# Optimization experiments

Hardware: AMD Instinct MI355X
Metric: run time of the kernel (lower is better)

Reference implementation:

```python
import jax, jax.numpy as jnp
import numpy as np

N_NODES = 50000
N_EDGES = 800000
D_IN = 96
D_HID = 96
N_CLASSES = 10
N_LAYERS = 3
BN_EPS = 1e-5


def setup_inputs() -> dict:
    key = jax.random.key(0)
    ks = jax.random.split(key, 10)
    x = jax.random.normal(ks[0], (N_NODES, D_IN), dtype=jnp.float32)
    edge_index = jax.random.randint(ks[1], (2, N_EDGES), 0, N_NODES, dtype=jnp.int64)
    s = 1.0 / np.sqrt(D_HID)
    # stacked per-layer params (in_channels == hidden_channels == 96)
    w_neigh = jax.random.normal(ks[2], (N_LAYERS, D_HID, D_HID), dtype=jnp.float32) * s
    w_self = jax.random.normal(ks[3], (N_LAYERS, D_HID, D_HID), dtype=jnp.float32) * s
    bias = jnp.zeros((N_LAYERS, D_HID), dtype=jnp.float32)
    bn_gamma = jnp.ones((N_LAYERS, D_HID), dtype=jnp.float32)
    bn_beta = jnp.zeros((N_LAYERS, D_HID), dtype=jnp.float32)
    clf_w = jax.random.normal(ks[4], (D_HID, N_CLASSES), dtype=jnp.float32) * s
    clf_b = jnp.zeros((N_CLASSES,), dtype=jnp.float32)
    return {"x": x, "edge_index": edge_index, "w_neigh": w_neigh,
            "w_self": w_self, "bias": bias, "bn_gamma": bn_gamma,
            "bn_beta": bn_beta, "clf_w": clf_w, "clf_b": clf_b}


def reference(x, edge_index, w_neigh, w_self, bias, bn_gamma, bn_beta, clf_w, clf_b):
    n = x.shape[0]
    src, dst = edge_index[0], edge_index[1]
    # in-degree per dst node (mean aggregation denominator), zero-deg -> 1
    deg = jax.ops.segment_sum(jnp.ones((src.shape[0],), x.dtype), dst, num_segments=n)
    inv_deg = (1.0 / jnp.maximum(deg, 1.0))[:, None]  # [N,1]
    h = x
    for i in range(N_LAYERS):
        # SAGEConv: mean-aggregate neighbor features, then lin_l(agg) + lin_r(self)
        agg = jax.ops.segment_sum(h[src], dst, num_segments=n) * inv_deg  # [N,D]
        h = agg @ w_neigh[i] + h @ w_self[i] + bias[i]
        # BatchNorm over nodes (batch statistics), then ReLU; dropout = identity (eval)
        mu = jnp.mean(h, axis=0)
        var = jnp.var(h, axis=0)
        h = (h - mu) * jax.lax.rsqrt(var + BN_EPS) * bn_gamma[i] + bn_beta[i]
        h = jax.nn.relu(h)
    return h @ clf_w + clf_b  # [N, num_classes]
```

## Files before the change

### kernel.cpp

```cpp
#include <hip/hip_runtime.h>

#define NN 50000
#define NE 800000
#define D 96
#define NL 3
#define NC 10
#define BN_EPS 1e-5f
#define INV_N (1.0f / (float)NN)
#define NB 196
#define CAP 6144
#define EPB 2048
#define NREP 16
#define WPAD 200
#define AGGU 16
#define CASTB ((NN * D / 4 + 255) / 256)
#define PREPWB ((NL * D * 192 + 255) / 256)

typedef short bf16x8 __attribute__((ext_vector_type(8)));
typedef unsigned short u16x8 __attribute__((ext_vector_type(8)));
typedef float f32x4 __attribute__((ext_vector_type(4)));

__device__ __forceinline__ unsigned short f2b(float x) {
    unsigned int u = __float_as_uint(x);
    unsigned int r = (u + 0x7fffu + ((u >> 16) & 1u)) >> 16;
    return (unsigned short)r;
}
__device__ __forceinline__ float blo(unsigned int u) { return __uint_as_float(u << 16); }
__device__ __forceinline__ float bhi(unsigned int u) { return __uint_as_float(u & 0xffff0000u); }
__device__ __forceinline__ float b2f(short s) {
    return __uint_as_float(((unsigned int)(unsigned short)s) << 16);
}
__device__ __forceinline__ unsigned int pk2(float lo, float hi) {
    return ((unsigned int)f2b(lo)) | (((unsigned int)f2b(hi)) << 16);
}

__device__ __forceinline__ int edge_at(const void* idx, int is64, long long pos) {
    if (is64) return (int)((const long long*)idx)[pos];
    return ((const int*)idx)[pos];
}

__global__ void __launch_bounds__(256) prep_kernel(
        const float* __restrict__ x, unsigned short* __restrict__ xb,
        const float* __restrict__ wn, const float* __restrict__ ws,
        unsigned short* __restrict__ wt,
        const int* __restrict__ words, int* __restrict__ flag,
        int* __restrict__ cnt, float* __restrict__ stats) {
    int b = blockIdx.x;
    int t = threadIdx.x;
    if (b < CASTB) {
        int i = b * 256 + t;
        if (i < NN * D / 4) {
            float4 v = ((const float4*)x)[i];
            ushort4 o;
            o.x = f2b(v.x); o.y = f2b(v.y); o.z = f2b(v.z); o.w = f2b(v.w);
            ((ushort4*)xb)[i] = o;
        }
        return;
    }
    if (b < CASTB + PREPWB) {
        int i = (b - CASTB) * 256 + t;
        if (i < NL * D * 192) {
            int k = i % 192;
            int col = (i / 192) % D;
            int l = i / (192 * D);
            float v = (k < D) ? wn[(size_t)l * D * D + k * D + col]
                              : ws[(size_t)l * D * D + (k - D) * D + col];
            wt[((size_t)l * D + col) * WPAD + k] = f2b(v);
        }
        return;
    }
    __shared__ int any_nz;
    if (t == 0) any_nz = 0;
    __syncthreads();
    if (words[2 * t + 1] != 0) atomicOr(&any_nz, 1);
    __syncthreads();
    if (t == 0) *flag = any_nz ? 0 : 1;
    if (t < NB) cnt[t] = 0;
    for (int i = t; i < NL * NREP * 2 * D; i += 256) stats[i] = 0.f;
}

__global__ void __launch_bounds__(256) bin_kernel(
        const void* __restrict__ idx, const int* __restrict__ flag,
        int* __restrict__ cnt, unsigned int* __restrict__ binned, int E) {
    __shared__ int hist[256];
    __shared__ int gbase[256];
    __shared__ unsigned int pk[EPB];
    __shared__ unsigned char bkt[EPB];
    int t = threadIdx.x;
    int base = blockIdx.x * EPB;
    int is64 = *flag;
    hist[t] = 0;
    __syncthreads();
    #pragma unroll
    for (int j = 0; j < 8; ++j) {
        int i = t + j * 256;
        int e = base + i;
        if (e < E) {
            int s = edge_at(idx, is64, e);
            int d = edge_at(idx, is64, (long long)E + e);
            int b = d >> 8;
            bkt[i] = (unsigned char)b;
            pk[i] = ((unsigned int)s << 8) | (unsigned int)(d & 255);
            atomicAdd(&hist[b], 1);
        } else {
            bkt[i] = 0xFF;
        }
    }
    __syncthreads();
    int h = hist[t];
    int gb = 0;
    if (t < NB && h > 0) gb = atomicAdd(&cnt[t], h);
    gbase[t] = gb;
    hist[t] = 0;
    __syncthreads();
    #pragma unroll
    for (int j = 0; j < 8; ++j) {
        int i = t + j * 256;
        int b = bkt[i];
        if (b != 0xFF) {
            int loc = atomicAdd(&hist[b], 1);
            int pos = gbase[b] + loc;
            if (pos < CAP) binned[(size_t)b * CAP + pos] = pk[i];
        }
    }
}

__global__ void __launch_bounds__(256) fill_bucket_kernel(
        const unsigned int* __restrict__ binned, const int* __restrict__ cnt,
        int* __restrict__ row_ptr, float* __restrict__ inv_deg,
        int* __restrict__ csr_src) {
    __shared__ int sexcl[256];
    __shared__ int deg_l[256];
    __shared__ int wsum[4];
    __shared__ int lds_csr[CAP];
    int b = blockIdx.x;
    int t = threadIdx.x;
    int lane = t & 63, w = t >> 6;
    {
        int v = (t < NB) ? cnt[t] : 0;
        int x = v;
        #pragma unroll
        for (int off = 1; off < 64; off <<= 1) {
            int y = __shfl_up(x, off);
            if (lane >= off) x += y;
        }
        if (lane == 63) wsum[w] = x;
        __syncthreads();
        if (t == 0) {
            int r = 0;
            #pragma unroll
            for (int i = 0; i < 4; ++i) { int tt = wsum[i]; wsum[i] = r; r += tt; }
        }
        __syncthreads();
        sexcl[t] = x - v + wsum[w];
        __syncthreads();
    }
    int base = sexcl[b];
    int count = cnt[b]; if (count > CAP) count = CAP;
    int n0 = b << 8;
    deg_l[t] = 0;
    __syncthreads();
    const unsigned int* reg = binned + (size_t)b * CAP;
    for (int i = t; i < count; i += 256) atomicAdd(&deg_l[reg[i] & 255], 1);
    __syncthreads();
    int v = deg_l[t];
    int x = v;
    #pragma unroll
    for (int off = 1; off < 64; off <<= 1) {
        int y = __shfl_up(x, off);
        if (lane >= off) x += y;
    }
    if (lane == 63) wsum[w] = x;
    __syncthreads();
    if (t == 0) {
        int r = 0;
        #pragma unroll
        for (int i = 0; i < 4; ++i) { int tt = wsum[i]; wsum[i] = r; r += tt; }
    }
    __syncthreads();
    int excl = x - v + wsum[w];
    int node = n0 + t;
    if (node < NN) {
        row_ptr[node] = base + excl;
        inv_deg[node] = 1.0f / (float)(v > 0 ? v : 1);
    }
    if (b == 0 && t == 0) row_ptr[NN] = NE;
    deg_l[t] = excl;
    __syncthreads();
    for (int i = t; i < count; i += 256) {
        unsigned int pkv = reg[i];
        int loc = atomicAdd(&deg_l[pkv & 255], 1);
        lds_csr[loc] = (int)(pkv >> 8);
    }
    __syncthreads();
    for (int i = t; i < count; i += 256) csr_src[base + i] = lds_csr[i];
}

__global__ void bn_coef_kernel(const float* __restrict__ stats,
                               const float* __restrict__ gamma,
                               const float* __restrict__ beta,
                               float* __restrict__ scsh) {
    int f = threadIdx.x;
    if (f >= D) return;
    float s = 0.f, q = 0.f;
    #pragma unroll
    for (int r = 0; r < NREP; ++r) {
        s += stats[r * 2 * D + f];
        q += stats[r * 2 * D + D + f];
    }
    float mu = s * INV_N;
    float va = q * INV_N - mu * mu;
    float sc = rsqrtf(va + BN_EPS) * gamma[f];
    scsh[f] = sc;
    scsh[D + f] = beta[f] - mu * sc;
}

__global__ void agg_kernel(const unsigned short* __restrict__ hb,
                           const int* __restrict__ row_ptr,
                           const int* __restrict__ csr_src,
                           const float* __restrict__ inv_deg,
                           unsigned short* __restrict__ aggb,
                           const float* __restrict__ scsh_in,
                           int use_bn, int n) {
    int gid = blockIdx.x * blockDim.x + threadIdx.x;
    int node = gid >> 6;
    int lane = gid & 63;
    if (node >= n) return;
    bool act = lane < 48;
    float sc0 = 1.f, sh0 = 0.f, sc1 = 1.f, sh1 = 0.f;
    float lo = use_bn ? 0.f : -3.0e38f;
    if (use_bn && act) {
        float2 scp = *(const float2*)(scsh_in + lane * 2);
        float2 shp = *(const float2*)(scsh_in + D + lane * 2);
        sc0 = scp.x; sc1 = scp.y; sh0 = shp.x; sh1 = shp.y;
    }
    int beg = row_ptr[node], end = row_ptr[node + 1];
    float a0 = 0.f, a1 = 0.f, b0 = 0.f, b1 = 0.f;
    float c0 = 0.f, c1 = 0.f, d0 = 0.f, d1 = 0.f;

    int e = beg;
    int sidx[AGGU];
    #pragma unroll
    for (int j = 0; j < AGGU; ++j) sidx[j] = (e + j < end) ? csr_src[e + j] : -1;
    while (e < end) {
        int enext = e + AGGU;
        int snext[AGGU];
        #pragma unroll
        for (int j = 0; j < AGGU; ++j)
            snext[j] = (enext + j < end) ? csr_src[enext + j] : -1;
        unsigned int u[AGGU];
        #pragma unroll
        for (int j = 0; j < AGGU; ++j) {
            int s = sidx[j];
            u[j] = (s >= 0 && act)
                 ? *(const unsigned int*)(hb + (size_t)s * D + lane * 2) : 0u;
        }
        #pragma unroll
        for (int j = 0; j < AGGU; ++j) {
            if (sidx[j] >= 0) {
                float x0 = fmaxf(fmaf(blo(u[j]), sc0, sh0), lo);
                float x1 = fmaxf(fmaf(bhi(u[j]), sc1, sh1), lo);
                if ((j & 3) == 0) { a0 += x0; a1 += x1; }
                else if ((j & 3) == 1) { b0 += x0; b1 += x1; }
                else if ((j & 3) == 2) { c0 += x0; c1 += x1; }
                else { d0 += x0; d1 += x1; }
            }
        }
        #pragma unroll
        for (int j = 0; j < AGGU; ++j) sidx[j] = snext[j];
        e = enext;
    }
    a0 = (a0 + b0) + (c0 + d0);
    a1 = (a1 + b1) + (c1 + d1);
    if (act) {
        float idg = inv_deg[node];
        *(unsigned int*)(aggb + (size_t)node * D + lane * 2) = pk2(a0 * idg, a1 * idg);
    }
}

__global__ void __launch_bounds__(256) mfma_gemm_kernel(
        const unsigned short* __restrict__ aggb,
        const unsigned short* __restrict__ hb,
        const unsigned short* __restrict__ wt,
        const float* __restrict__ bias,
        unsigned short* __restrict__ hout,
        float* __restrict__ stats,
        const float* __restrict__ scsh_in,
        int use_bn, int n) {
    __shared__ float red[4][192];
    __shared__ float sSC[D];
    __shared__ float sSH[D];
    __shared__ unsigned short sW[D][WPAD];
    int tid = threadIdx.x;
    int wave = tid >> 6;
    int lane = tid & 63;
    int m16 = lane & 15;
    int hi = lane >> 4;
    int rbase = blockIdx.x * 64 + wave * 16;

    int arow = rbase + m16;
    int arowc = arow < n ? arow : n - 1;
    const unsigned short* ap = aggb + (size_t)arowc * D + hi * 8;
    const unsigned short* hp = hb + (size_t)arowc * D + hi * 8;
    bf16x8 A[6], H[3];
    #pragma unroll
    for (int kk = 0; kk < 3; ++kk) A[kk] = *reinterpret_cast<const bf16x8*>(ap + kk * 32);
    #pragma unroll
    for (int kk = 0; kk < 3; ++kk) H[kk] = *reinterpret_cast<const bf16x8*>(hp + kk * 32);

    #pragma unroll
    for (int c = 0; c < 9; ++c) {
        int i = tid + c * 256;
        int col = i / 24, seg = i % 24;
        *reinterpret_cast<u16x8*>(&sW[col][seg * 8]) =
            *reinterpret_cast<const u16x8*>(wt + (size_t)col * WPAD + seg * 8);
    }

    if (use_bn && tid < D) {
        sSC[tid] = scsh_in[tid];
        sSH[tid] = scsh_in[D + tid];
    }
    __syncthreads();

    #pragma unroll
    for (int kk = 0; kk < 3; ++kk) {
        if (use_bn) {
            bf16x8 T;
            #pragma unroll
            for (int j = 0; j < 8; ++j) {
                int f = kk * 32 + hi * 8 + j;
                float v = fmaxf(fmaf(b2f(H[kk][j]), sSC[f], sSH[f]), 0.f);
                T[j] = (short)f2b(v);
            }
            A[3 + kk] = T;
        } else {
            A[3 + kk] = H[kk];
        }
    }

    f32x4 acc[6];
    #pragma unroll
    for (int nn = 0; nn < 6; ++nn) acc[nn] = (f32x4){0.f, 0.f, 0.f, 0.f};
    #pragma unroll
    for (int nn = 0; nn < 6; ++nn) {
        int col = nn * 16 + m16;
        #pragma unroll
        for (int kk = 0; kk < 6; ++kk) {
            bf16x8 B = *reinterpret_cast<const bf16x8*>(&sW[col][kk * 32 + hi * 8]);
            acc[nn] = __builtin_amdgcn_mfma_f32_16x16x32_bf16(A[kk], B, acc[nn], 0, 0, 0);
        }
    }

    #pragma unroll
    for (int nn = 0; nn < 6; ++nn) {
        int f = nn * 16 + m16;
        float bv = bias[f];
        float s = 0.f, q = 0.f;
        #pragma unroll
        for (int r = 0; r < 4; ++r) {
            int rrow = rbase + hi * 4 + r;
            float v = acc[nn][r] + bv;
            if (rrow < n) {
                hout[(size_t)rrow * D + f] = f2b(v);
                s += v;
                q += v * v;
            }
        }
        s += __shfl_xor(s, 16); q += __shfl_xor(q, 16);
        s += __shfl_xor(s, 32); q += __shfl_xor(q, 32);
        if (lane < 16) {
            red[wave][f] = s;
            red[wave][96 + f] = q;
        }
    }
    __syncthreads();
    if (tid < 192) {
        float t = red[0][tid] + red[1][tid] + red[2][tid] + red[3][tid];
        atomicAdd(&stats[(blockIdx.x & (NREP - 1)) * 2 * D + tid], t);
    }
}

__global__ void clf_kernel(const unsigned short* __restrict__ h,
                           const float* __restrict__ W,
                           const float* __restrict__ b,
                           const float* __restrict__ scsh_in,
                           float* __restrict__ out, int n) {
    __shared__ float sW[D * NC];
    __shared__ float sB[NC];
    __shared__ float sSC[D];
    __shared__ float sSH[D];
    int tid = threadIdx.x;
    for (int i = tid; i < D * NC; i += blockDim.x) sW[i] = W[i];
    if (tid < NC) sB[tid] = b[tid];
    if (tid < D) {
        sSC[tid] = scsh_in[tid];
        sSH[tid] = scsh_in[D + tid];
    }
    __syncthreads();
    int node = blockIdx.x * blockDim.x + tid;
    if (node >= n) return;
    float acc[NC];
    #pragma unroll
    for (int c = 0; c < NC; ++c) acc[c] = sB[c];
    const uint4* row = (const uint4*)(h + (size_t)node * D);
    #pragma unroll
    for (int q4 = 0; q4 < D / 8; ++q4) {
        uint4 v = row[q4];
        unsigned int* pv = (unsigned int*)&v;
        #pragma unroll
        for (int j = 0; j < 4; ++j) {
            int k = q4 * 8 + j * 2;
            float x0 = fmaxf(fmaf(blo(pv[j]), sSC[k], sSH[k]), 0.f);
            float x1 = fmaxf(fmaf(bhi(pv[j]), sSC[k + 1], sSH[k + 1]), 0.f);
            #pragma unroll
            for (int c = 0; c < NC; ++c)
                acc[c] += x0 * sW[k * NC + c] + x1 * sW[(k + 1) * NC + c];
        }
    }
    float* orow = out + (size_t)node * NC;
    #pragma unroll
    for (int c = 0; c < NC; ++c) orow[c] = acc[c];
}

extern "C" void kernel_launch(void* const* d_in, const int* in_sizes, int n_in,
                              void* d_out, int out_size, void* d_ws, size_t ws_size,
                              hipStream_t stream) {
    const float* x      = (const float*)d_in[0];
    const void*  eidx   = d_in[1];
    const float* w_ngh  = (const float*)d_in[2];
    const float* w_self = (const float*)d_in[3];
    const float* bias   = (const float*)d_in[4];
    const float* gamma  = (const float*)d_in[5];
    const float* beta   = (const float*)d_in[6];
    const float* clf_w  = (const float*)d_in[7];
    const float* clf_b  = (const float*)d_in[8];
    float* out = (float*)d_out;

    char* ws = (char*)d_ws;
    size_t o = 0;
    auto alloc = [&](size_t bytes) -> void* {
        void* r = ws + o;
        o += (bytes + 255) & ~(size_t)255;
        return r;
    };
    int*   flag    = (int*)alloc(4);
    int*   row_ptr = (int*)alloc((size_t)(NN + 1) * 4);
    float* inv_deg = (float*)alloc((size_t)NN * 4);
    int*   csr_src = (int*)alloc((size_t)NE * 4);
    float* stats   = (float*)alloc((size_t)NL * NREP * 2 * D * 4);
    float* scsh    = (float*)alloc((size_t)NL * 2 * D * 4);
    int*   cnt     = (int*)alloc((size_t)NB * 4);
    unsigned short* wt   = (unsigned short*)alloc((size_t)NL * D * WPAD * 2);
    unsigned short* xb   = (unsigned short*)alloc((size_t)NN * D * 2);
    unsigned short* aggb = (unsigned short*)alloc((size_t)NN * D * 2);
    unsigned short* hA   = (unsigned short*)alloc((size_t)NN * D * 2);
    unsigned short* hB   = (unsigned short*)alloc((size_t)NN * D * 2);
    unsigned int* binned = (unsigned int*)hA;

    prep_kernel<<<CASTB + PREPWB + 1, 256, 0, stream>>>(
        x, xb, w_ngh, w_self, wt, (const int*)eidx, flag, cnt, stats);
    bin_kernel<<<(NE + EPB - 1) / EPB, 256, 0, stream>>>(eidx, flag, cnt, binned, NE);
    fill_bucket_kernel<<<NB, 256, 0, stream>>>(binned, cnt, row_ptr, inv_deg, csr_src);

    const unsigned short* hin = xb;
    unsigned short* bufs[2] = {hA, hB};
    for (int l = 0; l < NL; ++l) {
        unsigned short* hout = bufs[l & 1];
        const float* coef_in = scsh + (size_t)(l - 1) * 2 * D;
        int use_bn = (l > 0) ? 1 : 0;
        if (!use_bn) coef_in = scsh;
        agg_kernel<<<(NN * 64 + 255) / 256, 256, 0, stream>>>(
            hin, row_ptr, csr_src, inv_deg, aggb, coef_in, use_bn, NN);
        mfma_gemm_kernel<<<(NN + 63) / 64, 256, 0, stream>>>(
            aggb, hin, wt + (size_t)l * D * WPAD, bias + (size_t)l * D,
            hout, stats + (size_t)l * NREP * 2 * D, coef_in, use_bn, NN);
        bn_coef_kernel<<<1, D, 0, stream>>>(stats + (size_t)l * NREP * 2 * D,
                                            gamma + (size_t)l * D, beta + (size_t)l * D,
                                            scsh + (size_t)l * 2 * D);
        hin = hout;
    }
    clf_kernel<<<(NN + 255) / 256, 256, 0, stream>>>(
        hin, clf_w, clf_b, scsh + (size_t)2 * 2 * D, out, NN);
}
```

Before: 205.8 us.

## Switch activations to fp16 with packed-half aggregation and separate BN-apply pass

Stores activations and weights as fp16 instead of bf16 and uses the f16 MFMA. The gather aggregation now sums in packed half2 arithmetic, with 16 lanes per edge across 4 edge groups, then reduces across groups with shuffles. BatchNorm+ReLU moves out of the aggregation, GEMM and classifier into a dedicated elementwise kernel per layer. This is meant to cut per-edge normalisation work and float conversions in the gather, but it adds an extra read/write pass per layer and risks precision loss or overflow when accumulating in fp16 over high-degree nodes.

Result: faster. 192.4 us (-6.5%).

```diff
diff --git a/kernel.cpp b/kernel.cpp
--- a/kernel.cpp
+++ b/kernel.cpp
@@ -12,26 +12,28 @@
 #define EPB 2048
 #define NREP 16
 #define WPAD 200
-#define AGGU 16
 #define CASTB ((NN * D / 4 + 255) / 256)
 #define PREPWB ((NL * D * 192 + 255) / 256)
 
-typedef short bf16x8 __attribute__((ext_vector_type(8)));
+typedef _Float16 f16x8 __attribute__((ext_vector_type(8)));
+typedef _Float16 h2t __attribute__((ext_vector_type(2)));
 typedef unsigned short u16x8 __attribute__((ext_vector_type(8)));
+typedef unsigned int u32x3 __attribute__((ext_vector_type(3)));
 typedef float f32x4 __attribute__((ext_vector_type(4)));
 
-__device__ __forceinline__ unsigned short f2b(float x) {
-    unsigned int u = __float_as_uint(x);
-    unsigned int r = (u + 0x7fffu + ((u >> 16) & 1u)) >> 16;
-    return (unsigned short)r;
-}
-__device__ __forceinline__ float blo(unsigned int u) { return __uint_as_float(u << 16); }
-__device__ __forceinline__ float bhi(unsigned int u) { return __uint_as_float(u & 0xffff0000u); }
-__device__ __forceinline__ float b2f(short s) {
-    return __uint_as_float(((unsigned int)(unsigned short)s) << 16);
-}
-__device__ __forceinline__ unsigned int pk2(float lo, float hi) {
-    return ((unsigned int)f2b(lo)) | (((unsigned int)f2b(hi)) << 16);
+__device__ __forceinline__ unsigned short f2h(float x) {
+    _Float16 h = (_Float16)x;
+    return __builtin_bit_cast(unsigned short, h);
+}
+__device__ __forceinline__ unsigned int pkh2(float lo, float hi) {
+    auto r = __builtin_amdgcn_cvt_pkrtz(lo, hi);
+    return __builtin_bit_cast(unsigned int, r);
+}
+__device__ __forceinline__ unsigned int pkadd(unsigned int a, unsigned int b) {
+    h2t x = __builtin_bit_cast(h2t, a);
+    h2t y = __builtin_bit_cast(h2t, b);
+    h2t z = x + y;
+    return __builtin_bit_cast(unsigned int, z);
 }
 
 __device__ __forceinline__ int edge_at(const void* idx, int is64, long long pos) {
@@ -52,7 +54,7 @@
         if (i < NN * D / 4) {
             float4 v = ((const float4*)x)[i];
             ushort4 o;
-            o.x = f2b(v.x); o.y = f2b(v.y); o.z = f2b(v.z); o.w = f2b(v.w);
+            o.x = f2h(v.x); o.y = f2h(v.y); o.z = f2h(v.z); o.w = f2h(v.w);
             ((ushort4*)xb)[i] = o;
         }
         return;
@@ -65,7 +67,7 @@
             int l = i / (192 * D);
             float v = (k < D) ? wn[(size_t)l * D * D + k * D + col]
                               : ws[(size_t)l * D * D + (k - D) * D + col];
-            wt[((size_t)l * D + col) * WPAD + k] = f2b(v);
+            wt[((size_t)l * D + col) * WPAD + k] = f2h(v);
         }
         return;
     }
@@ -215,66 +217,81 @@
     scsh[D + f] = beta[f] - mu * sc;
 }
 
+__global__ void __launch_bounds__(256) bn_apply_kernel(
+        const unsigned short* __restrict__ hpre,
+        const float* __restrict__ scsh,
+        unsigned short* __restrict__ hpost) {
+    __shared__ float sC[2 * D];
+    int t = threadIdx.x;
+    if (t < 2 * D) sC[t] = scsh[t];
+    __syncthreads();
+    int i = blockIdx.x * 256 + t;
+    if (i >= NN * D / 8) return;
+    uint4 v = ((const uint4*)hpre)[i];
+    int f0 = (i * 8) % D;
+    unsigned int* pv = (unsigned int*)&v;
+    uint4 o;
+    unsigned int* po = (unsigned int*)&o;
+    #pragma unroll
+    for (int j = 0; j < 4; ++j) {
+        int f = f0 + 2 * j;
+        h2t a = __builtin_bit_cast(h2t, pv[j]);
+        float x0 = fmaxf(fmaf((float)a.x, sC[f], sC[D + f]), 0.f);
+        float x1 = fmaxf(fmaf((float)a.y, sC[f + 1], sC[D + f + 1]), 0.f);
+        po[j] = pkh2(x0, x1);
+    }
+    ((uint4*)hpost)[i] = o;
+}
+
 __global__ void agg_kernel(const unsigned short* __restrict__ hb,
                            const int* __restrict__ row_ptr,
                            const int* __restrict__ csr_src,
                            const float* __restrict__ inv_deg,
-                           unsigned short* __restrict__ aggb,
-                           const float* __restrict__ scsh_in,
-                           int use_bn, int n) {
+                           unsigned short* __restrict__ aggb, int n) {
     int gid = blockIdx.x * blockDim.x + threadIdx.x;
     int node = gid >> 6;
     int lane = gid & 63;
     if (node >= n) return;
-    bool act = lane < 48;
-    float sc0 = 1.f, sh0 = 0.f, sc1 = 1.f, sh1 = 0.f;
-    float lo = use_bn ? 0.f : -3.0e38f;
-    if (use_bn && act) {
-        float2 scp = *(const float2*)(scsh_in + lane * 2);
-        float2 shp = *(const float2*)(scsh_in + D + lane * 2);
-        sc0 = scp.x; sc1 = scp.y; sh0 = shp.x; sh1 = shp.y;
-    }
+    int g = lane >> 4;
+    unsigned int p12 = (lane & 15) * 12u;
     int beg = row_ptr[node], end = row_ptr[node + 1];
-    float a0 = 0.f, a1 = 0.f, b0 = 0.f, b1 = 0.f;
-    float c0 = 0.f, c1 = 0.f, d0 = 0.f, d1 = 0.f;
-
+    const char* hbase = (const char*)hb;
+
+    u32x3 acc0 = {0, 0, 0}, acc1 = {0, 0, 0};
     int e = beg;
-    int sidx[AGGU];
-    #pragma unroll
-    for (int j = 0; j < AGGU; ++j) sidx[j] = (e + j < end) ? csr_src[e + j] : -1;
+    int i0 = (beg + g < end) ? csr_src[beg + g] : -1;
+    int i1 = (beg + 4 + g < end) ? csr_src[beg + 4 + g] : -1;
     while (e < end) {
-        int enext = e + AGGU;
-        int snext[AGGU];
-        #pragma unroll
-        for (int j = 0; j < AGGU; ++j)
-            snext[j] = (enext + j < end) ? csr_src[enext + j] : -1;
-        unsigned int u[AGGU];
-        #pragma unroll
-        for (int j = 0; j < AGGU; ++j) {
-            int s = sidx[j];
-            u[j] = (s >= 0 && act)
-                 ? *(const unsigned int*)(hb + (size_t)s * D + lane * 2) : 0u;
-        }
-        #pragma unroll
-        for (int j = 0; j < AGGU; ++j) {
-            if (sidx[j] >= 0) {
-                float x0 = fmaxf(fmaf(blo(u[j]), sc0, sh0), lo);
-                float x1 = fmaxf(fmaf(bhi(u[j]), sc1, sh1), lo);
-                if ((j & 3) == 0) { a0 += x0; a1 += x1; }
-                else if ((j & 3) == 1) { b0 += x0; b1 += x1; }
-                else if ((j & 3) == 2) { c0 += x0; c1 += x1; }
-                else { d0 += x0; d1 += x1; }
-            }
-        }
-        #pragma unroll
-        for (int j = 0; j < AGGU; ++j) sidx[j] = snext[j];
-        e = enext;
-    }
-    a0 = (a0 + b0) + (c0 + d0);
-    a1 = (a1 + b1) + (c1 + d1);
-    if (act) {
+        u32x3 u0 = {0, 0, 0}, u1 = {0, 0, 0};
+        if (i0 >= 0) u0 = *(const u32x3*)(hbase + (unsigned)i0 * 192u + p12);
+        if (i1 >= 0) u1 = *(const u32x3*)(hbase + (unsigned)i1 * 192u + p12);
+        int en = e + 8;
+        i0 = (en + g < end) ? csr_src[en + g] : -1;
+        i1 = (en + 4 + g < end) ? csr_src[en + 4 + g] : -1;
+        #pragma unroll
+        for (int r = 0; r < 3; ++r) {
+            acc0[r] = pkadd(acc0[r], u0[r]);
+            acc1[r] = pkadd(acc1[r], u1[r]);
+        }
+        e = en;
+    }
+    unsigned int acc[3];
+    #pragma unroll
+    for (int r = 0; r < 3; ++r) {
+        unsigned int a = pkadd(acc0[r], acc1[r]);
+        a = pkadd(a, (unsigned int)__shfl_xor((int)a, 16));
+        a = pkadd(a, (unsigned int)__shfl_xor((int)a, 32));
+        acc[r] = a;
+    }
+    if (lane < 16) {
         float idg = inv_deg[node];
-        *(unsigned int*)(aggb + (size_t)node * D + lane * 2) = pk2(a0 * idg, a1 * idg);
+        u32x3 o;
+        #pragma unroll
+        for (int r = 0; r < 3; ++r) {
+            h2t a = __builtin_bit_cast(h2t, acc[r]);
+            o[r] = pkh2((float)a.x * idg, (float)a.y * idg);
+        }
+        *(u32x3*)((char*)aggb + (unsigned)node * 192u + p12) = o;
     }
 }
 
@@ -285,11 +302,8 @@
         const float* __restrict__ bias,
         unsigned short* __restrict__ hout,
         float* __restrict__ stats,
-        const float* __restrict__ scsh_in,
-        int use_bn, int n) {
+        int n) {
     __shared__ float red[4][192];
-    __shared__ float sSC[D];
-    __shared__ float sSH[D];
     __shared__ unsigned short sW[D][WPAD];
     int tid = threadIdx.x;
     int wave = tid >> 6;
@@ -302,11 +316,11 @@
     int arowc = arow < n ? arow : n - 1;
     const unsigned short* ap = aggb + (size_t)arowc * D + hi * 8;
     const unsigned short* hp = hb + (size_t)arowc * D + hi * 8;
-    bf16x8 A[6], H[3];
-    #pragma unroll
-    for (int kk = 0; kk < 3; ++kk) A[kk] = *reinterpret_cast<const bf16x8*>(ap + kk * 32);
-    #pragma unroll
-    for (int kk = 0; kk < 3; ++kk) H[kk] = *reinterpret_cast<const bf16x8*>(hp + kk * 32);
+    f16x8 A[6];
+    #pragma unroll
+    for (int kk = 0; kk < 3; ++kk) A[kk] = *reinterpret_cast<const f16x8*>(ap + kk * 32);
+    #pragma unroll
+    for (int kk = 0; kk < 3; ++kk) A[3 + kk] = *reinterpret_cast<const f16x8*>(hp + kk * 32);
 
     #pragma unroll
     for (int c = 0; c < 9; ++c) {
@@ -315,28 +329,7 @@
         *reinterpret_cast<u16x8*>(&sW[col][seg * 8]) =
             *reinterpret_cast<const u16x8*>(wt + (size_t)col * WPAD + seg * 8);
     }
-
-    if (use_bn && tid < D) {
-        sSC[tid] = scsh_in[tid];
-        sSH[tid] = scsh_in[D + tid];
-    }
-    __syncthreads();
-
-    #pragma unroll
-    for (int kk = 0; kk < 3; ++kk) {
-        if (use_bn) {
-            bf16x8 T;
-            #pragma unroll
-            for (int j = 0; j < 8; ++j) {
-                int f = kk * 32 + hi * 8 + j;
-                float v = fmaxf(fmaf(b2f(H[kk][j]), sSC[f], sSH[f]), 0.f);
-                T[j] = (short)f2b(v);
-            }
-            A[3 + kk] = T;
-        } else {
-            A[3 + kk] = H[kk];
-        }
-    }
+    __syncthreads();
 
     f32x4 acc[6];
     #pragma unroll
@@ -346,8 +339,8 @@
         int col = nn * 16 + m16;
         #pragma unroll
         for (int kk = 0; kk < 6; ++kk) {
-            bf16x8 B = *reinterpret_cast<const bf16x8*>(&sW[col][kk * 32 + hi * 8]);
-            acc[nn] = __builtin_amdgcn_mfma_f32_16x16x32_bf16(A[kk], B, acc[nn], 0, 0, 0);
+            f16x8 B = *reinterpret_cast<const f16x8*>(&sW[col][kk * 32 + hi * 8]);
+            acc[nn] = __builtin_amdgcn_mfma_f32_16x16x32_f16(A[kk], B, acc[nn], 0, 0, 0);
         }
     }
 
@@ -361,7 +354,7 @@
             int rrow = rbase + hi * 4 + r;
             float v = acc[nn][r] + bv;
             if (rrow < n) {
-                hout[(size_t)rrow * D + f] = f2b(v);
+                hout[(size_t)rrow * D + f] = f2h(v);
                 s += v;
                 q += v * v;
             }
@@ -383,19 +376,12 @@
 __global__ void clf_kernel(const unsigned short* __restrict__ h,
                            const float* __restrict__ W,
                            const float* __restrict__ b,
-                           const float* __restrict__ scsh_in,
                            float* __restrict__ out, int n) {
     __shared__ float sW[D * NC];
     __shared__ float sB[NC];
-    __shared__ float sSC[D];
-    __shared__ float sSH[D];
     int tid = threadIdx.x;
     for (int i = tid; i < D * NC; i += blockDim.x) sW[i] = W[i];
     if (tid < NC) sB[tid] = b[tid];
-    if (tid < D) {
-        sSC[tid] = scsh_in[tid];
-        sSH[tid] = scsh_in[D + tid];
-    }
     __syncthreads();
     int node = blockIdx.x * blockDim.x + tid;
     if (node >= n) return;
@@ -410,8 +396,9 @@
         #pragma unroll
         for (int j = 0; j < 4; ++j) {
             int k = q4 * 8 + j * 2;
-            float x0 = fmaxf(fmaf(blo(pv[j]), sSC[k], sSH[k]), 0.f);
-            float x1 = fmaxf(fmaf(bhi(pv[j]), sSC[k + 1], sSH[k + 1]), 0.f);
+            h2t a = __builtin_bit_cast(h2t, pv[j]);
+            float x0 = (float)a.x;
+            float x1 = (float)a.y;
             #pragma unroll
             for (int c = 0; c < NC; ++c)
                 acc[c] += x0 * sW[k * NC + c] + x1 * sW[(k + 1) * NC + c];
@@ -453,9 +440,10 @@
     unsigned short* wt   = (unsigned short*)alloc((size_t)NL * D * WPAD * 2);
     unsigned short* xb   = (unsigned short*)alloc((size_t)NN * D * 2);
     unsigned short* aggb = (unsigned short*)alloc((size_t)NN * D * 2);
-    unsigned short* hA   = (unsigned short*)alloc((size_t)NN * D * 2);
-    unsigned short* hB   = (unsigned short*)alloc((size_t)NN * D * 2);
-    unsigned int* binned = (unsigned int*)hA;
+    unsigned short* hpre = (unsigned short*)alloc((size_t)NN * D * 2);
+    unsigned short* hpA  = (unsigned short*)alloc((size_t)NN * D * 2);
+    unsigned short* hpB  = (unsigned short*)alloc((size_t)NN * D * 2);
+    unsigned int* binned = (unsigned int*)hpA;
 
     prep_kernel<<<CASTB + PREPWB + 1, 256, 0, stream>>>(
         x, xb, w_ngh, w_self, wt, (const int*)eidx, flag, cnt, stats);
@@ -463,22 +451,19 @@
     fill_bucket_kernel<<<NB, 256, 0, stream>>>(binned, cnt, row_ptr, inv_deg, csr_src);
 
     const unsigned short* hin = xb;
-    unsigned short* bufs[2] = {hA, hB};
+    unsigned short* hpost[NL] = {hpA, hpB, hpA};
     for (int l = 0; l < NL; ++l) {
-        unsigned short* hout = bufs[l & 1];
-        const float* coef_in = scsh + (size_t)(l - 1) * 2 * D;
-        int use_bn = (l > 0) ? 1 : 0;
-        if (!use_bn) coef_in = scsh;
         agg_kernel<<<(NN * 64 + 255) / 256, 256, 0, stream>>>(
-            hin, row_ptr, csr_src, inv_deg, aggb, coef_in, use_bn, NN);
+            hin, row_ptr, csr_src, inv_deg, aggb, NN);
         mfma_gemm_kernel<<<(NN + 63) / 64, 256, 0, stream>>>(
             aggb, hin, wt + (size_t)l * D * WPAD, bias + (size_t)l * D,
-            hout, stats + (size_t)l * NREP * 2 * D, coef_in, use_bn, NN);
+            hpre, stats + (size_t)l * NREP * 2 * D, NN);
         bn_coef_kernel<<<1, D, 0, stream>>>(stats + (size_t)l * NREP * 2 * D,
                                             gamma + (size_t)l * D, beta + (size_t)l * D,
                                             scsh + (size_t)l * 2 * D);
-        hin = hout;
-    }
-    clf_kernel<<<(NN + 255) / 256, 256, 0, stream>>>(
-        hin, clf_w, clf_b, scsh + (size_t)2 * 2 * D, out, NN);
-}
+        bn_apply_kernel<<<(NN * D / 8 + 255) / 256, 256, 0, stream>>>(
+            hpre, scsh + (size_t)l * 2 * D, hpost[l]);
+        hin = hpost[l];
+    }
+    clf_kernel<<<(NN + 255) / 256, 256, 0, stream>>>(hin, clf_w, clf_b, out, NN);
+}
```
